# Kernel tuning notes

Hardware: AMD Instinct MI355X
Metric: run time of the kernel (lower is better)

The kernel has to match this reference:

```python
import jax, jax.numpy as jnp
import numpy as np


def setup_inputs() -> dict:
    key = jax.random.key(0)
    ks = jax.random.split(key, 13)
    B, T, D = 512, 256, 64
    H, G = 256, 192          # encoder hidden, lifted dim
    L = D + G                # ldim = 256
    s = lambda n: 1.0 / np.sqrt(n)
    return {
        "x": jax.random.normal(ks[0], (B, T, D), jnp.float32),
        "u": jax.random.normal(ks[1], (B, T, D), jnp.float32),
        "Wx1": jax.random.normal(ks[2], (D, H), jnp.float32) * s(D),
        "bx1": jax.random.normal(ks[3], (H,), jnp.float32) * 0.01,
        "Wx2": jax.random.normal(ks[4], (H, H), jnp.float32) * s(H),
        "bx2": jax.random.normal(ks[5], (H,), jnp.float32) * 0.01,
        "Wx3": jax.random.normal(ks[6], (H, G), jnp.float32) * s(H),
        "Wu1": jax.random.normal(ks[7], (D, H), jnp.float32) * s(D),
        "bu1": jax.random.normal(ks[8], (H,), jnp.float32) * 0.01,
        "Wu2": jax.random.normal(ks[9], (H, G), jnp.float32) * s(H),
        "WB": jax.random.normal(ks[10], (D + G, L), jnp.float32) * s(D + G),
        "WK": jax.random.normal(ks[11], (L, L), jnp.float32) * s(L),
        "bK": jax.random.normal(ks[12], (L,), jnp.float32) * 0.01,
        "n_shifts": 256,
    }


def reference(x, u, Wx1, bx1, Wx2, bx2, Wx3, Wu1, bu1, Wu2, WB, WK, bK, n_shifts):
    x = x[:, :n_shifts, :]
    u = u[:, :n_shifts, :]
    # encoder_x: relu(Linear) -> relu(Linear) -> Linear(no bias), dropout p=0 is identity
    g = jnp.maximum(x @ Wx1 + bx1, 0.0)
    g = jnp.maximum(g @ Wx2 + bx2, 0.0)
    g = g @ Wx3
    y = jnp.concatenate([x, g], axis=-1)          # [B, T, ldim]
    # encoder_u: relu(Linear) -> Linear(no bias)
    v = jnp.maximum(u @ Wu1 + bu1, 0.0) @ Wu2
    uu = jnp.concatenate([u, v], axis=-1)         # [B, T, D+G]
    Bu = uu @ WB                                  # [B, T, ldim]
    # Koopman linear recurrence: y_{t+1} = K y_t + bK + Bu_t
    y0 = y[:, 0, :]                               # [B, ldim]

    def step(carry, bu_t):
        y_next = carry @ WK + bK + bu_t
        return y_next, y_next

    _, ys = jax.lax.scan(step, y0, jnp.swapaxes(Bu[:, :-1, :], 0, 1))  # [T-1, B, ldim]
    y_pred = jnp.concatenate([y0[:, None, :], jnp.swapaxes(ys, 0, 1)], axis=1)
    return (y, y_pred)
```

## Files before the change

kernel.cpp:

```cpp
#include <hip/hip_runtime.h>
#include <hip/hip_bf16.h>

#define MM 131072

typedef __attribute__((ext_vector_type(8))) short short8;
typedef __attribute__((ext_vector_type(4))) float f32x4;

#define GLP(p) (const __attribute__((address_space(1))) void*)(p)
#define LDSP(p) (__attribute__((address_space(3))) void*)(p)

static __device__ __forceinline__ unsigned short f2bf(float f) {
    union { float f; unsigned int u; } v; v.f = f;
    unsigned int r = v.u + 0x7FFF + ((v.u >> 16) & 1);
    return (unsigned short)(r >> 16);
}
static __device__ __forceinline__ float bf2f(unsigned short h) {
    union { float f; unsigned int u; } v; v.u = ((unsigned int)h) << 16;
    return v.f;
}

__global__ __launch_bounds__(256) void prepA(
    const float* __restrict__ x, const float* __restrict__ u,
    __hip_bfloat16* __restrict__ xb, __hip_bfloat16* __restrict__ ub,
    float* __restrict__ y,
    const float* __restrict__ W0, const float* __restrict__ W1,
    const float* __restrict__ W2, const float* __restrict__ W3,
    const float* __restrict__ W4, const float* __restrict__ W5,
    __hip_bfloat16* __restrict__ T0, __hip_bfloat16* __restrict__ T1,
    __hip_bfloat16* __restrict__ T2, __hip_bfloat16* __restrict__ T3,
    __hip_bfloat16* __restrict__ T4, __hip_bfloat16* __restrict__ T5,
    const float* __restrict__ WK, const float* __restrict__ WB,
    float* __restrict__ W2f, float* __restrict__ WBWf)
{
    __shared__ __align__(16) float As[16][68];
    __shared__ __align__(16) float Ws[16][64];

    if (blockIdx.x < 16384) {
        int i = blockIdx.x * 256 + threadIdx.x;
        const float* s; __hip_bfloat16* d; int j; bool isx;
        if (i < 2097152) { s = x; d = xb; j = i; isx = true; }
        else             { s = u; d = ub; j = i - 2097152; isx = false; }
        const float4 v = ((const float4*)s)[j];
        union { unsigned short h[4]; uint2 u2; } p;
        p.h[0] = f2bf(v.x); p.h[1] = f2bf(v.y);
        p.h[2] = f2bf(v.z); p.h[3] = f2bf(v.w);
        ((uint2*)d)[j] = p.u2;
        if (isx) {
            const int r = j >> 4, q = j & 15;
            ((float4*)(y + (size_t)r * 256))[q] = v;
        }
    } else if (blockIdx.x < 17408) {
        const int b = blockIdx.x - 16384;
        const float* W; __hip_bfloat16* T; int K, N, i0;
        if      (b < 64)  { W = W0; T = T0; K = 64;  N = 256; i0 = b; }
        else if (b < 320) { W = W1; T = T1; K = 256; N = 256; i0 = b - 64; }
        else if (b < 512) { W = W2; T = T2; K = 256; N = 192; i0 = b - 320; }
        else if (b < 576) { W = W3; T = T3; K = 64;  N = 256; i0 = b - 512; }
        else if (b < 768) { W = W4; T = T4; K = 256; N = 192; i0 = b - 576; }
        else              { W = W5; T = T5; K = 256; N = 256; i0 = b - 768; }
        const int i = i0 * 256 + threadIdx.x;
        if (i < K * N) {
            const int n = i / K, k = i - n * K;
            T[i] = __float2bfloat16(W[(size_t)k * N + n]);
        }
    } else {
        const int tile = blockIdx.x - 17408;
        const int e  = tile >> 4;
        const int tl = tile & 15;
        const float* A = e ? WB : WK;
        const float* W = WK;
        float*       C = e ? WBWf : W2f;
        const int row0 = (tl >> 2) * 64;
        const int col0 = (tl & 3) * 64;
        const int tx = threadIdx.x & 15;
        const int ty = threadIdx.x >> 4;
        float acc[4][4] = {};
        for (int k0 = 0; k0 < 256; k0 += 16) {
            {
                const int kk = threadIdx.x & 15;
                const int r  = threadIdx.x >> 4;
                #pragma unroll
                for (int rr = 0; rr < 4; ++rr)
                    As[kk][r + rr * 16] = A[(size_t)(row0 + r + rr * 16) * 256 + k0 + kk];
            }
            {
                const int n  = threadIdx.x & 63;
                const int kz = threadIdx.x >> 6;
                #pragma unroll
                for (int kq = 0; kq < 4; ++kq) {
                    const int kk = kz + kq * 4;
                    Ws[kk][n] = W[(size_t)(k0 + kk) * 256 + col0 + n];
                }
            }
            __syncthreads();
            #pragma unroll
            for (int kk = 0; kk < 16; ++kk) {
                const float4 a4 = *(const float4*)&As[kk][ty * 4];
                const float4 w4 = *(const float4*)&Ws[kk][tx * 4];
                const float av[4] = {a4.x, a4.y, a4.z, a4.w};
                const float wv[4] = {w4.x, w4.y, w4.z, w4.w};
                #pragma unroll
                for (int i = 0; i < 4; ++i)
                    #pragma unroll
                    for (int j = 0; j < 4; ++j)
                        acc[i][j] += av[i] * wv[j];
            }
            __syncthreads();
        }
        #pragma unroll
        for (int i = 0; i < 4; ++i)
            #pragma unroll
            for (int j = 0; j < 4; ++j)
                C[(size_t)(row0 + ty * 4 + i) * 256 + col0 + tx * 4 + j] = acc[i][j];
    }
}

struct G5 { const float* a[5]; const float* b[5]; float* c[5]; };

__global__ __launch_bounds__(256) void wgemm(G5 P)
{
    __shared__ __align__(16) float As[16][68];
    __shared__ __align__(16) float Ws[16][64];

    const int e  = blockIdx.x >> 4;
    const int tl = blockIdx.x & 15;
    const float* A = P.a[e];
    const float* W = P.b[e];
    float*       C = P.c[e];
    const int row0 = (tl >> 2) * 64;
    const int col0 = (tl & 3) * 64;

    const int tx = threadIdx.x & 15;
    const int ty = threadIdx.x >> 4;

    float acc[4][4] = {};

    for (int k0 = 0; k0 < 256; k0 += 16) {
        {
            const int kk = threadIdx.x & 15;
            const int r  = threadIdx.x >> 4;
            #pragma unroll
            for (int rr = 0; rr < 4; ++rr)
                As[kk][r + rr * 16] = A[(size_t)(row0 + r + rr * 16) * 256 + k0 + kk];
        }
        {
            const int n  = threadIdx.x & 63;
            const int kz = threadIdx.x >> 6;
            #pragma unroll
            for (int kq = 0; kq < 4; ++kq) {
                const int kk = kz + kq * 4;
                Ws[kk][n] = W[(size_t)(k0 + kk) * 256 + col0 + n];
            }
        }
        __syncthreads();
        #pragma unroll
        for (int kk = 0; kk < 16; ++kk) {
            const float4 a4 = *(const float4*)&As[kk][ty * 4];
            const float4 w4 = *(const float4*)&Ws[kk][tx * 4];
            const float av[4] = {a4.x, a4.y, a4.z, a4.w};
            const float wv[4] = {w4.x, w4.y, w4.z, w4.w};
            #pragma unroll
            for (int i = 0; i < 4; ++i)
                #pragma unroll
                for (int j = 0; j < 4; ++j)
                    acc[i][j] += av[i] * wv[j];
        }
        __syncthreads();
    }

    #pragma unroll
    for (int i = 0; i < 4; ++i)
        #pragma unroll
        for (int j = 0; j < 4; ++j)
            C[(size_t)(row0 + ty * 4 + i) * 256 + col0 + tx * 4 + j] = acc[i][j];
}

__global__ __launch_bounds__(512) void ffC(
    const __hip_bfloat16* __restrict__ x_bf,
    const __hip_bfloat16* __restrict__ u_bf,
    const __hip_bfloat16* __restrict__ Wx1T, const float* __restrict__ bx1,
    const __hip_bfloat16* __restrict__ Wx2T, const float* __restrict__ bx2,
    const __hip_bfloat16* __restrict__ Wx3T,
    const __hip_bfloat16* __restrict__ Wu1T, const float* __restrict__ bu1,
    const __hip_bfloat16* __restrict__ Wu2T,
    float* __restrict__ y, __hip_bfloat16* __restrict__ vout,
    const float* __restrict__ WB, const float* __restrict__ WBW,
    const float* __restrict__ WBW2, const float* __restrict__ WBW3,
    __hip_bfloat16* __restrict__ T4,
    const float* __restrict__ bK, const float* __restrict__ WK,
    const float* __restrict__ W2f, const float* __restrict__ W3f,
    float* __restrict__ cK4)
{
    __shared__ __align__(16) __hip_bfloat16 I[128 * 256];
    __shared__ __align__(16) __hip_bfloat16 Bs[256 * 32];
    __shared__ __align__(16) __hip_bfloat16 As[128 * 32];

    const int tid  = threadIdx.x;

    if (blockIdx.x >= 2048) {
        if (blockIdx.x < 2560) {
            const int o = (blockIdx.x - 2048) * 512 + tid;
            const int n = o >> 10;
            const int rem = o & 1023;
            const int j = rem >> 8, k = rem & 255;
            const float* src = (j == 0) ? WB : (j == 1) ? WBW : (j == 2) ? WBW2 : WBW3;
            ((unsigned short*)T4)[o] = f2bf(src[(size_t)k * 256 + n]);
        } else {
            if (tid < 256) {
                const int col = tid;
                float s = bK[col];
                for (int k = 0; k < 256; ++k)
                    s += bK[k] * (WK[(size_t)k * 256 + col] + W2f[(size_t)k * 256 + col]
                                  + W3f[(size_t)k * 256 + col]);
                cK4[col] = s;
            }
        }
        return;
    }

    const bool isx = blockIdx.x < 1024;
    const __hip_bfloat16* in  = isx ? x_bf : u_bf;
    const __hip_bfloat16* W1T = isx ? Wx1T : Wu1T;
    const float*          b1  = isx ? bx1  : bu1;
    const int lane = tid & 63;
    const int wid  = tid >> 6;
    const int wm   = wid & 1;
    const int wn   = wid >> 1;
    const int row0 = (blockIdx.x & 1023) * 128;
    const int rlow = lane & 15;
    const int c    = lane >> 4;

    f32x4 acc[4][4];
    #pragma unroll
    for (int mi = 0; mi < 4; ++mi)
        #pragma unroll
        for (int ni = 0; ni < 4; ++ni)
            acc[mi][ni] = {0.f, 0.f, 0.f, 0.f};

    for (int k0 = 0; k0 < 64; k0 += 32) {
        {
            const int i = tid;
            const int row = i >> 2;
            const int cl  = (i & 3) ^ ((row >> 1) & 3);
            __builtin_amdgcn_global_load_lds(
                GLP(in + (size_t)(row0 + row) * 64 + k0 + cl * 8),
                LDSP(As + i * 8), 16, 0, 0);
        }
        #pragma unroll
        for (int r = 0; r < 2; ++r) {
            const int i = r * 512 + tid;
            const int row = i >> 2;
            const int cl  = (i & 3) ^ ((row >> 1) & 3);
            __builtin_amdgcn_global_load_lds(
                GLP(W1T + (size_t)row * 64 + k0 + cl * 8),
                LDSP(Bs + i * 8), 16, 0, 0);
        }
        __syncthreads();
        short8 af[4], bfr[4];
        #pragma unroll
        for (int mi = 0; mi < 4; ++mi) {
            const int row  = wm * 64 + mi * 16 + rlow;
            const int phys = c ^ ((row >> 1) & 3);
            af[mi] = *(const short8*)((const char*)As + row * 64 + phys * 16);
        }
        #pragma unroll
        for (int ni = 0; ni < 4; ++ni) {
            const int row  = wn * 64 + ni * 16 + rlow;
            const int phys = c ^ ((row >> 1) & 3);
            bfr[ni] = *(const short8*)((const char*)Bs + row * 64 + phys * 16);
        }
        #pragma unroll
        for (int mi = 0; mi < 4; ++mi)
            #pragma unroll
            for (int ni = 0; ni < 4; ++ni)
                acc[mi][ni] = __builtin_amdgcn_mfma_f32_16x16x32_bf16(
                    af[mi], bfr[ni], acc[mi][ni], 0, 0, 0);
        __syncthreads();
    }
    #pragma unroll
    for (int ni = 0; ni < 4; ++ni) {
        const int col = wn * 64 + ni * 16 + rlow;
        const float bv = b1[col];
        #pragma unroll
        for (int mi = 0; mi < 4; ++mi)
            #pragma unroll
            for (int q = 0; q < 4; ++q) {
                const int row = wm * 64 + mi * 16 + c * 4 + q;
                const int byte = (row * 512 + col * 2) ^ ((row & 7) << 4);
                *(unsigned short*)((char*)I + byte) = f2bf(fmaxf(acc[mi][ni][q] + bv, 0.f));
            }
    }
    __syncthreads();

    if (isx) {
        #pragma unroll
        for (int mi = 0; mi < 4; ++mi)
            #pragma unroll
            for (int ni = 0; ni < 4; ++ni)
                acc[mi][ni] = {0.f, 0.f, 0.f, 0.f};

        for (int k0 = 0; k0 < 256; k0 += 32) {
            #pragma unroll
            for (int r = 0; r < 2; ++r) {
                const int i = r * 512 + tid;
                const int row = i >> 2;
                const int cl  = (i & 3) ^ ((row >> 1) & 3);
                __builtin_amdgcn_global_load_lds(
                    GLP(Wx2T + (size_t)row * 256 + k0 + cl * 8),
                    LDSP(Bs + i * 8), 16, 0, 0);
            }
            __syncthreads();
            short8 af[4], bfr[4];
            #pragma unroll
            for (int mi = 0; mi < 4; ++mi) {
                const int row = wm * 64 + mi * 16 + rlow;
                const int off = (row * 512 + k0 * 2 + c * 16) ^ ((row & 7) << 4);
                af[mi] = *(const short8*)((const char*)I + off);
            }
            #pragma unroll
            for (int ni = 0; ni < 4; ++ni) {
                const int row  = wn * 64 + ni * 16 + rlow;
                const int phys = c ^ ((row >> 1) & 3);
                bfr[ni] = *(const short8*)((const char*)Bs + row * 64 + phys * 16);
            }
            #pragma unroll
            for (int mi = 0; mi < 4; ++mi)
                #pragma unroll
                for (int ni = 0; ni < 4; ++ni)
                    acc[mi][ni] = __builtin_amdgcn_mfma_f32_16x16x32_bf16(
                        af[mi], bfr[ni], acc[mi][ni], 0, 0, 0);
            __syncthreads();
        }
        #pragma unroll
        for (int ni = 0; ni < 4; ++ni) {
            const int col = wn * 64 + ni * 16 + rlow;
            const float bv = bx2[col];
            #pragma unroll
            for (int mi = 0; mi < 4; ++mi)
                #pragma unroll
                for (int q = 0; q < 4; ++q) {
                    const int row = wm * 64 + mi * 16 + c * 4 + q;
                    const int byte = (row * 512 + col * 2) ^ ((row & 7) << 4);
                    *(unsigned short*)((char*)I + byte) = f2bf(fmaxf(acc[mi][ni][q] + bv, 0.f));
                }
        }
        __syncthreads();
    }

    const __hip_bfloat16* WfT = isx ? Wx3T : Wu2T;
    f32x4 a3[4][3];
    #pragma unroll
    for (int mi = 0; mi < 4; ++mi)
        #pragma unroll
        for (int ni = 0; ni < 3; ++ni)
            a3[mi][ni] = {0.f, 0.f, 0.f, 0.f};

    for (int k0 = 0; k0 < 256; k0 += 32) {
        #pragma unroll
        for (int r = 0; r < 2; ++r) {
            const int i = r * 512 + tid;
            if (i < 768) {
                const int row = i >> 2;
                const int cl  = (i & 3) ^ ((row >> 1) & 3);
                __builtin_amdgcn_global_load_lds(
                    GLP(WfT + (size_t)row * 256 + k0 + cl * 8),
                    LDSP(Bs + i * 8), 16, 0, 0);
            }
        }
        __syncthreads();
        short8 af[4], bfr[3];
        #pragma unroll
        for (int mi = 0; mi < 4; ++mi) {
            const int row = wm * 64 + mi * 16 + rlow;
            const int off = (row * 512 + k0 * 2 + c * 16) ^ ((row & 7) << 4);
            af[mi] = *(const short8*)((const char*)I + off);
        }
        #pragma unroll
        for (int ni = 0; ni < 3; ++ni) {
            const int row  = wn * 48 + ni * 16 + rlow;
            const int phys = c ^ ((row >> 1) & 3);
            bfr[ni] = *(const short8*)((const char*)Bs + row * 64 + phys * 16);
        }
        #pragma unroll
        for (int mi = 0; mi < 4; ++mi)
            #pragma unroll
            for (int ni = 0; ni < 3; ++ni)
                a3[mi][ni] = __builtin_amdgcn_mfma_f32_16x16x32_bf16(
                    af[mi], bfr[ni], a3[mi][ni], 0, 0, 0);
        __syncthreads();
    }
    #pragma unroll
    for (int ni = 0; ni < 3; ++ni) {
        const int col = wn * 48 + ni * 16 + rlow;
        #pragma unroll
        for (int mi = 0; mi < 4; ++mi)
            #pragma unroll
            for (int q = 0; q < 4; ++q) {
                const int row = row0 + wm * 64 + mi * 16 + c * 4 + q;
                if (isx) y[(size_t)row * 256 + 64 + col] = a3[mi][ni][q];
                else     ((unsigned short*)vout)[(size_t)row * 192 + col] = f2bf(a3[mi][ni][q]);
            }
    }
}

__global__ __launch_bounds__(256) void d4gS(
    const __hip_bfloat16* __restrict__ u_bf, const __hip_bfloat16* __restrict__ v,
    const __hip_bfloat16* __restrict__ WBT4, const float* __restrict__ cK4,
    float* __restrict__ yp,
    const __hip_bfloat16* __restrict__ WBT, const float* __restrict__ bK,
    float* __restrict__ stash)
{
    __shared__ __align__(16) __hip_bfloat16 As[132 * 32];
    __shared__ __align__(16) __hip_bfloat16 Bs[4][128 * 32];

    const int tid  = threadIdx.x;

    if (blockIdx.x >= 2048) {
        float* uuL = (float*)As;
        const int b = blockIdx.x - 2048;
        #pragma unroll
        for (int p = 0; p < 3; ++p) {
            float val;
            if (tid < 64) val = bf2f(((const unsigned short*)u_bf)[((size_t)b * 256 + p) * 64 + tid]);
            else          val = bf2f(((const unsigned short*)v)[((size_t)b * 256 + p) * 192 + tid - 64]);
            uuL[p * 256 + tid] = val;
        }
        __syncthreads();
        const int col = tid;
        float a0 = bK[col], a1 = a0, a2 = a0;
        for (int k = 0; k < 256; ++k) {
            const float w = bf2f(((const unsigned short*)WBT)[(size_t)col * 256 + k]);
            a0 += uuL[0 * 256 + k] * w;
            a1 += uuL[1 * 256 + k] * w;
            a2 += uuL[2 * 256 + k] * w;
        }
        stash[((size_t)b * 3 + 0) * 256 + col] = a0;
        stash[((size_t)b * 3 + 1) * 256 + col] = a1;
        stash[((size_t)b * 3 + 2) * 256 + col] = a2;
        return;
    }

    const int lane = tid & 63;
    const int wid  = tid >> 6;
    const int wm   = wid & 1;
    const int wn   = wid >> 1;
    const int row0 = (blockIdx.x >> 1) * 128;
    const int col0 = (blockIdx.x & 1) * 128;
    const int rlow = lane & 15;
    const int c    = lane >> 4;

    f32x4 acc[4][4];
    #pragma unroll
    for (int mi = 0; mi < 4; ++mi)
        #pragma unroll
        for (int ni = 0; ni < 4; ++ni)
            acc[mi][ni] = {0.f, 0.f, 0.f, 0.f};

    for (int kl = 0; kl < 256; kl += 32) {
        const __hip_bfloat16* Ab; int Al, kk;
        if (kl < 64) { Ab = u_bf; Al = 64;  kk = kl; }
        else         { Ab = v;    Al = 192; kk = kl - 64; }

        #pragma unroll
        for (int r = 0; r < 3; ++r) {
            const int i = r * 256 + tid;
            if (i < 528) {
                const int row = i >> 2;
                const int cl  = (i & 3) ^ ((row >> 1) & 3);
                int srow = row0 - 4 + row;
                if (srow < 0) srow = 0;
                __builtin_amdgcn_global_load_lds(
                    GLP(Ab + (size_t)srow * Al + kk + cl * 8),
                    LDSP(As + i * 8), 16, 0, 0);
            }
        }
        #pragma unroll
        for (int r = 0; r < 8; ++r) {
            const int i = r * 256 + tid;
            const int j = i >> 9;
            const int s = i & 511;
            const int row = s >> 2;
            const int cl  = (s & 3) ^ ((row >> 1) & 3);
            __builtin_amdgcn_global_load_lds(
                GLP(WBT4 + (size_t)(col0 + row) * 1024 + j * 256 + kl + cl * 8),
                LDSP(&Bs[0][0] + i * 8), 16, 0, 0);
        }
        __syncthreads();

        #pragma unroll
        for (int j = 0; j < 4; ++j) {
            short8 bfr[4];
            #pragma unroll
            for (int ni = 0; ni < 4; ++ni) {
                const int row  = wn * 64 + ni * 16 + rlow;
                const int phys = c ^ ((row >> 1) & 3);
                bfr[ni] = *(const short8*)((const char*)Bs[j] + row * 64 + phys * 16);
            }
            #pragma unroll
            for (int mi = 0; mi < 4; ++mi) {
                const int prow = wm * 64 + mi * 16 + rlow + 3 - j;
                const int phys = c ^ ((prow >> 1) & 3);
                const short8 af = *(const short8*)((const char*)As + prow * 64 + phys * 16);
                #pragma unroll
                for (int ni = 0; ni < 4; ++ni)
                    acc[mi][ni] = __builtin_amdgcn_mfma_f32_16x16x32_bf16(
                        af, bfr[ni], acc[mi][ni], 0, 0, 0);
            }
        }
        __syncthreads();
    }

    const int q4 = lane >> 4;
    #pragma unroll
    for (int ni = 0; ni < 4; ++ni) {
        const int col = col0 + wn * 64 + ni * 16 + rlow;
        const float bv = cK4[col];
        #pragma unroll
        for (int mi = 0; mi < 4; ++mi) {
            #pragma unroll
            for (int q = 0; q < 4; ++q) {
                const int row = row0 + wm * 64 + mi * 16 + q4 * 4 + q;
                if ((row & 255) >= 4)
                    yp[(size_t)row * 256 + col] = acc[mi][ni][q] + bv;
            }
        }
    }
}

static __device__ __forceinline__ void gather_frags(
    const float* __restrict__ M, int col0, int rlow, int kg,
    short8 (&wh)[2][8], short8 (&wl)[2][8])
{
    #pragma unroll
    for (int tile = 0; tile < 2; ++tile) {
        const int col = col0 + tile * 16 + rlow;
        for (int kc = 0; kc < 8; ++kc) {
            const int k0 = kc * 32 + kg * 8;
            short8 h, l;
            for (int i = 0; i < 8; ++i) {
                const float w = M[(size_t)(k0 + i) * 256 + col];
                const unsigned short hb = f2bf(w);
                h[i] = (short)hb;
                l[i] = (short)f2bf(w - bf2f(hb));
            }
            wh[tile][kc] = h;
            wl[tile][kc] = l;
        }
    }
}

__global__ __launch_bounds__(512, 1) void scan4(
    const float* __restrict__ WK, const float* __restrict__ W4,
    const float* __restrict__ stash,
    const float* __restrict__ y, float* __restrict__ yp)
{
    __shared__ __align__(16) __hip_bfloat16 cbuf[2][2][16 * 256];

    const int tid  = threadIdx.x;
    const int lane = tid & 63;
    const int wid  = tid >> 6;
    const int b0   = blockIdx.x * 4;
    const int col0 = wid * 32;
    const int rlow = lane & 15;
    const int kg   = lane >> 4;
    const int rswz = (rlow & 7) << 4;

    #pragma unroll
    for (int e = 0; e < 2; ++e) {
        const int idx = tid * 2 + e;
        const int br  = idx >> 8;
        const int cc  = idx & 255;
        const float v = y[(size_t)(b0 + br) * 65536 + cc];
        yp[(size_t)(b0 + br) * 65536 + cc] = v;
        const unsigned short hb = f2bf(v);
        const unsigned short lb = f2bf(v - bf2f(hb));
        const int byte = (br * 512 + cc * 2) ^ ((br & 7) << 4);
        *(unsigned short*)((char*)&cbuf[0][0][0] + byte) = hb;
        *(unsigned short*)((char*)&cbuf[0][1][0] + byte) = lb;
    }
    __syncthreads();

    short8 wh[2][8], wl[2][8];
    gather_frags(WK, col0, rlow, kg, wh, wl);

    for (int p = 1; p < 4; ++p) {
        f32x4 aHH[2], aHL[2], aLH[2];
        #pragma unroll
        for (int tile = 0; tile < 2; ++tile) {
            aHH[tile] = {0.f, 0.f, 0.f, 0.f};
            aHL[tile] = {0.f, 0.f, 0.f, 0.f};
            aLH[tile] = {0.f, 0.f, 0.f, 0.f};
        }
        const char* hbase = (const char*)&cbuf[0][0][0];
        const char* lbase = (const char*)&cbuf[0][1][0];
        #pragma unroll
        for (int kc = 0; kc < 8; ++kc) {
            const int off = (rlow * 512 + kg * 16 + kc * 64) ^ rswz;
            const short8 ah = *(const short8*)(hbase + off);
            const short8 al = *(const short8*)(lbase + off);
            aHH[0] = __builtin_amdgcn_mfma_f32_16x16x32_bf16(ah, wh[0][kc], aHH[0], 0, 0, 0);
            aHH[1] = __builtin_amdgcn_mfma_f32_16x16x32_bf16(ah, wh[1][kc], aHH[1], 0, 0, 0);
            aHL[0] = __builtin_amdgcn_mfma_f32_16x16x32_bf16(ah, wl[0][kc], aHL[0], 0, 0, 0);
            aHL[1] = __builtin_amdgcn_mfma_f32_16x16x32_bf16(ah, wl[1][kc], aHL[1], 0, 0, 0);
            aLH[0] = __builtin_amdgcn_mfma_f32_16x16x32_bf16(al, wh[0][kc], aLH[0], 0, 0, 0);
            aLH[1] = __builtin_amdgcn_mfma_f32_16x16x32_bf16(al, wh[1][kc], aLH[1], 0, 0, 0);
        }
        __builtin_amdgcn_sched_barrier(0);
        asm volatile("s_waitcnt lgkmcnt(0)" ::: "memory");
        __builtin_amdgcn_s_barrier();
        __builtin_amdgcn_sched_barrier(0);

        if (kg == p - 1) {
            #pragma unroll
            for (int tile = 0; tile < 2; ++tile) {
                const int col = col0 + tile * 16 + rlow;
                #pragma unroll
                for (int q = 0; q < 4; ++q) {
                    const float cv = stash[((size_t)(b0 + q) * 3 + (p - 1)) * 256 + col];
                    const float yv = aHH[tile][q] + aHL[tile][q] + aLH[tile][q] + cv;
                    const int wr = p * 4 + q;
                    const unsigned short hb = f2bf(yv);
                    const unsigned short lb = f2bf(yv - bf2f(hb));
                    const int byte = (wr * 512 + col * 2) ^ ((wr & 7) << 4);
                    *(unsigned short*)((char*)&cbuf[0][0][0] + byte) = hb;
                    *(unsigned short*)((char*)&cbuf[0][1][0] + byte) = lb;
                    yp[(size_t)(b0 + q) * 65536 + (size_t)p * 256 + col] = yv;
                }
            }
        }
        __builtin_amdgcn_sched_barrier(0);
        asm volatile("s_waitcnt lgkmcnt(0)" ::: "memory");
        __builtin_amdgcn_s_barrier();
        __builtin_amdgcn_sched_barrier(0);
    }

    gather_frags(W4, col0, rlow, kg, wh, wl);

    float dv[2][4];
    #pragma unroll
    for (int tile = 0; tile < 2; ++tile) {
        const int col = col0 + tile * 16 + rlow;
        #pragma unroll
        for (int q = 0; q < 4; ++q)
            dv[tile][q] = yp[(size_t)(b0 + q) * 65536 + (size_t)(4 + kg) * 256 + col];
    }

    int cur = 0;
    for (int s = 0; s < 63; ++s) {
        const int tb = 4 + s * 4;

        float dn[2][4];
        if (s < 62) {
            #pragma unroll
            for (int tile = 0; tile < 2; ++tile) {
                const int col = col0 + tile * 16 + rlow;
                #pragma unroll
                for (int q = 0; q < 4; ++q)
                    dn[tile][q] = yp[(size_t)(b0 + q) * 65536
                                     + (size_t)(tb + 4 + kg) * 256 + col];
            }
        }

        f32x4 aHH[2], aHL[2], aLH[2];
        #pragma unroll
        for (int tile = 0; tile < 2; ++tile) {
            aHH[tile] = {0.f, 0.f, 0.f, 0.f};
            aHL[tile] = {0.f, 0.f, 0.f, 0.f};
            aLH[tile] = {0.f, 0.f, 0.f, 0.f};
        }
        const char* hbase = (const char*)&cbuf[cur][0][0];
        const char* lbase = (const char*)&cbuf[cur][1][0];
        #pragma unroll
        for (int kc = 0; kc < 8; ++kc) {
            const int off = (rlow * 512 + kg * 16 + kc * 64) ^ rswz;
            const short8 ah = *(const short8*)(hbase + off);
            const short8 al = *(const short8*)(lbase + off);
            aHH[0] = __builtin_amdgcn_mfma_f32_16x16x32_bf16(ah, wh[0][kc], aHH[0], 0, 0, 0);
            aHH[1] = __builtin_amdgcn_mfma_f32_16x16x32_bf16(ah, wh[1][kc], aHH[1], 0, 0, 0);
            aHL[0] = __builtin_amdgcn_mfma_f32_16x16x32_bf16(ah, wl[0][kc], aHL[0], 0, 0, 0);
            aHL[1] = __builtin_amdgcn_mfma_f32_16x16x32_bf16(ah, wl[1][kc], aHL[1], 0, 0, 0);
            aLH[0] = __builtin_amdgcn_mfma_f32_16x16x32_bf16(al, wh[0][kc], aLH[0], 0, 0, 0);
            aLH[1] = __builtin_amdgcn_mfma_f32_16x16x32_bf16(al, wh[1][kc], aLH[1], 0, 0, 0);
        }

        char* whb = (char*)&cbuf[cur ^ 1][0][0];
        char* wlb = (char*)&cbuf[cur ^ 1][1][0];
        #pragma unroll
        for (int tile = 0; tile < 2; ++tile) {
            const int col = col0 + tile * 16 + rlow;
            #pragma unroll
            for (int q = 0; q < 4; ++q) {
                const int row = kg * 4 + q;
                const float yv = aHH[tile][q] + aHL[tile][q] + aLH[tile][q] + dv[tile][q];
                const unsigned short hb = f2bf(yv);
                const unsigned short lb = f2bf(yv - bf2f(hb));
                const int byte = (row * 512 + col * 2) ^ ((row & 7) << 4);
                *(unsigned short*)(whb + byte) = hb;
                *(unsigned short*)(wlb + byte) = lb;
                yp[(size_t)(b0 + q) * 65536 + (size_t)(tb + kg) * 256 + col] = yv;
            }
        }
        if (s < 62) {
            #pragma unroll
            for (int tile = 0; tile < 2; ++tile)
                #pragma unroll
                for (int q = 0; q < 4; ++q)
                    dv[tile][q] = dn[tile][q];
        }

        __builtin_amdgcn_sched_barrier(0);
        asm volatile("s_waitcnt lgkmcnt(0)" ::: "memory");
        __builtin_amdgcn_s_barrier();
        __builtin_amdgcn_sched_barrier(0);
        cur ^= 1;
    }
}

extern "C" void kernel_launch(void* const* d_in, const int* in_sizes, int n_in,
                              void* d_out, int out_size, void* d_ws, size_t ws_size,
                              hipStream_t stream)
{
    const float* x   = (const float*)d_in[0];
    const float* u   = (const float*)d_in[1];
    const float* Wx1 = (const float*)d_in[2];
    const float* bx1 = (const float*)d_in[3];
    const float* Wx2 = (const float*)d_in[4];
    const float* bx2 = (const float*)d_in[5];
    const float* Wx3 = (const float*)d_in[6];
    const float* Wu1 = (const float*)d_in[7];
    const float* bu1 = (const float*)d_in[8];
    const float* Wu2 = (const float*)d_in[9];
    const float* WB  = (const float*)d_in[10];
    const float* WK  = (const float*)d_in[11];
    const float* bK  = (const float*)d_in[12];

    float* y  = (float*)d_out;
    float* yp = y + (size_t)MM * 256;

    char* ws = (char*)d_ws;
    __hip_bfloat16* x_bf = (__hip_bfloat16*)(ws);
    __hip_bfloat16* u_bf = (__hip_bfloat16*)(ws + 16777216);
    __hip_bfloat16* wTb  = (__hip_bfloat16*)(ws + 33554432);
    __hip_bfloat16* Wx1T = wTb;
    __hip_bfloat16* Wx2T = wTb + 16384;
    __hip_bfloat16* Wx3T = wTb + 81920;
    __hip_bfloat16* Wu1T = wTb + 131072;
    __hip_bfloat16* Wu2T = wTb + 147456;
    __hip_bfloat16* WBT  = wTb + 196608;
    __hip_bfloat16* t2   = (__hip_bfloat16*)(ws + 34078720);
    float* W2f   = (float*)(ws + 101187584);
    float* W3f   = (float*)(ws + 101449728);
    float* W4f   = (float*)(ws + 101711872);
    float* WBWf  = (float*)(ws + 101974016);
    float* WBW2f = (float*)(ws + 102236160);
    float* WBW3f = (float*)(ws + 102498304);
    __hip_bfloat16* WBT4 = (__hip_bfloat16*)(ws + 102760448);
    float* cK4   = (float*)(ws + 103284736);
    float* stash = (float*)(ws + 103285760);

    prepA<<<17440, dim3(256), 0, stream>>>(x, u, x_bf, u_bf, y,
        Wx1, Wx2, Wx3, Wu1, Wu2, WB,
        Wx1T, Wx2T, Wx3T, Wu1T, Wu2T, WBT,
        WK, WB, W2f, WBWf);

    {
        G5 L2 = {{W2f, W2f, WBWf, WBWf, nullptr},
                 {WK, W2f, WK, W2f, nullptr},
                 {W3f, W4f, WBW2f, WBW3f, nullptr}};
        wgemm<<<64, dim3(256), 0, stream>>>(L2);
    }

    ffC<<<2561, dim3(512), 0, stream>>>(x_bf, u_bf,
        Wx1T, bx1, Wx2T, bx2, Wx3T, Wu1T, bu1, Wu2T,
        y, t2,
        WB, WBWf, WBW2f, WBW3f, WBT4,
        bK, WK, W2f, W3f, cK4);

    d4gS<<<2560, dim3(256), 0, stream>>>(u_bf, t2, WBT4, cK4, yp, WBT, bK, stash);

    scan4<<<128, dim3(512), 0, stream>>>(WK, W4f, stash, y, yp);
}
```

Measured before the change: 410.3 us.

## Load larger K tiles in encoder MLP and split recurrence MFMA accumulator chains

```diff
diff --git a/kernel.cpp b/kernel.cpp
--- a/kernel.cpp
+++ b/kernel.cpp
@@ -192,8 +192,8 @@
     float* __restrict__ cK4)
 {
     __shared__ __align__(16) __hip_bfloat16 I[128 * 256];
-    __shared__ __align__(16) __hip_bfloat16 Bs[256 * 32];
-    __shared__ __align__(16) __hip_bfloat16 As[128 * 32];
+    __shared__ __align__(16) __hip_bfloat16 Bs[256 * 128];
+    __shared__ __align__(16) __hip_bfloat16 As[128 * 64];
 
     const int tid  = threadIdx.x;
 
@@ -237,91 +237,40 @@
         for (int ni = 0; ni < 4; ++ni)
             acc[mi][ni] = {0.f, 0.f, 0.f, 0.f};
 
-    for (int k0 = 0; k0 < 64; k0 += 32) {
-        {
-            const int i = tid;
-            const int row = i >> 2;
-            const int cl  = (i & 3) ^ ((row >> 1) & 3);
-            __builtin_amdgcn_global_load_lds(
-                GLP(in + (size_t)(row0 + row) * 64 + k0 + cl * 8),
-                LDSP(As + i * 8), 16, 0, 0);
-        }
+    {
         #pragma unroll
         for (int r = 0; r < 2; ++r) {
             const int i = r * 512 + tid;
-            const int row = i >> 2;
-            const int cl  = (i & 3) ^ ((row >> 1) & 3);
+            const int row = i >> 3;
+            const int cl  = (i & 7) ^ (row & 7);
             __builtin_amdgcn_global_load_lds(
-                GLP(W1T + (size_t)row * 64 + k0 + cl * 8),
+                GLP(in + (size_t)(row0 + row) * 64 + cl * 8),
+                LDSP(As + i * 8), 16, 0, 0);
+        }
+        #pragma unroll
+        for (int r = 0; r < 4; ++r) {
+            const int i = r * 512 + tid;
+            const int row = i >> 3;
+            const int cl  = (i & 7) ^ (row & 7);
+            __builtin_amdgcn_global_load_lds(
+                GLP(W1T + (size_t)row * 64 + cl * 8),
                 LDSP(Bs + i * 8), 16, 0, 0);
         }
         __syncthreads();
-        short8 af[4], bfr[4];
-        #pragma unroll
-        for (int mi = 0; mi < 4; ++mi) {
-            const int row  = wm * 64 + mi * 16 + rlow;
-            const int phys = c ^ ((row >> 1) & 3);
-            af[mi] = *(const short8*)((const char*)As + row * 64 + phys * 16);
-        }
-        #pragma unroll
-        for (int ni = 0; ni < 4; ++ni) {
-            const int row  = wn * 64 + ni * 16 + rlow;
-            const int phys = c ^ ((row >> 1) & 3);
-            bfr[ni] = *(const short8*)((const char*)Bs + row * 64 + phys * 16);
-        }
-        #pragma unroll
-        for (int mi = 0; mi < 4; ++mi)
-            #pragma unroll
-            for (int ni = 0; ni < 4; ++ni)
-                acc[mi][ni] = __builtin_amdgcn_mfma_f32_16x16x32_bf16(
-                    af[mi], bfr[ni], acc[mi][ni], 0, 0, 0);
-        __syncthreads();
-    }
-    #pragma unroll
-    for (int ni = 0; ni < 4; ++ni) {
-        const int col = wn * 64 + ni * 16 + rlow;
-        const float bv = b1[col];
-        #pragma unroll
-        for (int mi = 0; mi < 4; ++mi)
-            #pragma unroll
-            for (int q = 0; q < 4; ++q) {
-                const int row = wm * 64 + mi * 16 + c * 4 + q;
-                const int byte = (row * 512 + col * 2) ^ ((row & 7) << 4);
-                *(unsigned short*)((char*)I + byte) = f2bf(fmaxf(acc[mi][ni][q] + bv, 0.f));
-            }
-    }
-    __syncthreads();
-
-    if (isx) {
-        #pragma unroll
-        for (int mi = 0; mi < 4; ++mi)
-            #pragma unroll
-            for (int ni = 0; ni < 4; ++ni)
-                acc[mi][ni] = {0.f, 0.f, 0.f, 0.f};
-
-        for (int k0 = 0; k0 < 256; k0 += 32) {
-            #pragma unroll
-            for (int r = 0; r < 2; ++r) {
-                const int i = r * 512 + tid;
-                const int row = i >> 2;
-                const int cl  = (i & 3) ^ ((row >> 1) & 3);
-                __builtin_amdgcn_global_load_lds(
-                    GLP(Wx2T + (size_t)row * 256 + k0 + cl * 8),
-                    LDSP(Bs + i * 8), 16, 0, 0);
-            }
-            __syncthreads();
+        #pragma unroll
+        for (int k0 = 0; k0 < 64; k0 += 32) {
             short8 af[4], bfr[4];
             #pragma unroll
             for (int mi = 0; mi < 4; ++mi) {
-                const int row = wm * 64 + mi * 16 + rlow;
-                const int off = (row * 512 + k0 * 2 + c * 16) ^ ((row & 7) << 4);
-                af[mi] = *(const short8*)((const char*)I + off);
+                const int row  = wm * 64 + mi * 16 + rlow;
+                const int phys = ((k0 >> 3) + c) ^ (row & 7);
+                af[mi] = *(const short8*)((const char*)As + row * 128 + phys * 16);
             }
             #pragma unroll
             for (int ni = 0; ni < 4; ++ni) {
                 const int row  = wn * 64 + ni * 16 + rlow;
-                const int phys = c ^ ((row >> 1) & 3);
-                bfr[ni] = *(const short8*)((const char*)Bs + row * 64 + phys * 16);
+                const int phys = ((k0 >> 3) + c) ^ (row & 7);
+                bfr[ni] = *(const short8*)((const char*)Bs + row * 128 + phys * 16);
             }
             #pragma unroll
             for (int mi = 0; mi < 4; ++mi)
@@ -329,16 +278,16 @@
                 for (int ni = 0; ni < 4; ++ni)
                     acc[mi][ni] = __builtin_amdgcn_mfma_f32_16x16x32_bf16(
                         af[mi], bfr[ni], acc[mi][ni], 0, 0, 0);
-            __syncthreads();
-        }
+        }
+        __syncthreads();
         #pragma unroll
         for (int ni = 0; ni < 4; ++ni) {
             const int col = wn * 64 + ni * 16 + rlow;
-            const float bv = bx2[col];
-            #pragma unroll
-            for (int mi = 0; mi < 4; ++mi)
-                #pragma unroll
-                for (int q = 0; q < 4; ++q) {
+            const float bv = b1[col];
+            #pragma unroll
+            for (int q = 0; q < 4; ++q)
+                #pragma unroll
+                for (int mi = 0; mi < 4; ++mi) {
                     const int row = wm * 64 + mi * 16 + c * 4 + q;
                     const int byte = (row * 512 + col * 2) ^ ((row & 7) << 4);
                     *(unsigned short*)((char*)I + byte) = f2bf(fmaxf(acc[mi][ni][q] + bv, 0.f));
@@ -347,6 +296,65 @@
         __syncthreads();
     }
 
+    if (isx) {
+        #pragma unroll
+        for (int mi = 0; mi < 4; ++mi)
+            #pragma unroll
+            for (int ni = 0; ni < 4; ++ni)
+                acc[mi][ni] = {0.f, 0.f, 0.f, 0.f};
+
+        for (int half = 0; half < 2; ++half) {
+            const int k0b = half * 128;
+            #pragma unroll
+            for (int r = 0; r < 8; ++r) {
+                const int i = r * 512 + tid;
+                const int row = i >> 4;
+                const int cl  = (i & 15) ^ (row & 7);
+                __builtin_amdgcn_global_load_lds(
+                    GLP(Wx2T + (size_t)row * 256 + k0b + cl * 8),
+                    LDSP(Bs + i * 8), 16, 0, 0);
+            }
+            __syncthreads();
+            #pragma unroll
+            for (int k0l = 0; k0l < 128; k0l += 32) {
+                short8 af[4], bfr[4];
+                #pragma unroll
+                for (int mi = 0; mi < 4; ++mi) {
+                    const int row = wm * 64 + mi * 16 + rlow;
+                    const int off = (row * 512 + (k0b + k0l) * 2 + c * 16) ^ ((row & 7) << 4);
+                    af[mi] = *(const short8*)((const char*)I + off);
+                }
+                #pragma unroll
+                for (int ni = 0; ni < 4; ++ni) {
+                    const int row  = wn * 64 + ni * 16 + rlow;
+                    const int phys = ((k0l >> 3) + c) ^ (row & 7);
+                    bfr[ni] = *(const short8*)((const char*)Bs + row * 256 + phys * 16);
+                }
+                #pragma unroll
+                for (int mi = 0; mi < 4; ++mi)
+                    #pragma unroll
+                    for (int ni = 0; ni < 4; ++ni)
+                        acc[mi][ni] = __builtin_amdgcn_mfma_f32_16x16x32_bf16(
+                            af[mi], bfr[ni], acc[mi][ni], 0, 0, 0);
+            }
+            __syncthreads();
+        }
+        #pragma unroll
+        for (int ni = 0; ni < 4; ++ni) {
+            const int col = wn * 64 + ni * 16 + rlow;
+            const float bv = bx2[col];
+            #pragma unroll
+            for (int q = 0; q < 4; ++q)
+                #pragma unroll
+                for (int mi = 0; mi < 4; ++mi) {
+                    const int row = wm * 64 + mi * 16 + c * 4 + q;
+                    const int byte = (row * 512 + col * 2) ^ ((row & 7) << 4);
+                    *(unsigned short*)((char*)I + byte) = f2bf(fmaxf(acc[mi][ni][q] + bv, 0.f));
+                }
+        }
+        __syncthreads();
+    }
+
     const __hip_bfloat16* WfT = isx ? Wx3T : Wu2T;
     f32x4 a3[4][3];
     #pragma unroll
@@ -355,38 +363,40 @@
         for (int ni = 0; ni < 3; ++ni)
             a3[mi][ni] = {0.f, 0.f, 0.f, 0.f};
 
-    for (int k0 = 0; k0 < 256; k0 += 32) {
-        #pragma unroll
-        for (int r = 0; r < 2; ++r) {
+    for (int half = 0; half < 2; ++half) {
+        const int k0b = half * 128;
+        #pragma unroll
+        for (int r = 0; r < 6; ++r) {
             const int i = r * 512 + tid;
-            if (i < 768) {
-                const int row = i >> 2;
-                const int cl  = (i & 3) ^ ((row >> 1) & 3);
-                __builtin_amdgcn_global_load_lds(
-                    GLP(WfT + (size_t)row * 256 + k0 + cl * 8),
-                    LDSP(Bs + i * 8), 16, 0, 0);
-            }
-        }
-        __syncthreads();
-        short8 af[4], bfr[3];
-        #pragma unroll
-        for (int mi = 0; mi < 4; ++mi) {
-            const int row = wm * 64 + mi * 16 + rlow;
-            const int off = (row * 512 + k0 * 2 + c * 16) ^ ((row & 7) << 4);
-            af[mi] = *(const short8*)((const char*)I + off);
-        }
-        #pragma unroll
-        for (int ni = 0; ni < 3; ++ni) {
-            const int row  = wn * 48 + ni * 16 + rlow;
-            const int phys = c ^ ((row >> 1) & 3);
-            bfr[ni] = *(const short8*)((const char*)Bs + row * 64 + phys * 16);
-        }
-        #pragma unroll
-        for (int mi = 0; mi < 4; ++mi)
-            #pragma unroll
-            for (int ni = 0; ni < 3; ++ni)
-                a3[mi][ni] = __builtin_amdgcn_mfma_f32_16x16x32_bf16(
-                    af[mi], bfr[ni], a3[mi][ni], 0, 0, 0);
+            const int row = i >> 4;
+            const int cl  = (i & 15) ^ (row & 7);
+            __builtin_amdgcn_global_load_lds(
+                GLP(WfT + (size_t)row * 256 + k0b + cl * 8),
+                LDSP(Bs + i * 8), 16, 0, 0);
+        }
+        __syncthreads();
+        #pragma unroll
+        for (int k0l = 0; k0l < 128; k0l += 32) {
+            short8 af[4], bfr[3];
+            #pragma unroll
+            for (int mi = 0; mi < 4; ++mi) {
+                const int row = wm * 64 + mi * 16 + rlow;
+                const int off = (row * 512 + (k0b + k0l) * 2 + c * 16) ^ ((row & 7) << 4);
+                af[mi] = *(const short8*)((const char*)I + off);
+            }
+            #pragma unroll
+            for (int ni = 0; ni < 3; ++ni) {
+                const int row  = wn * 48 + ni * 16 + rlow;
+                const int phys = ((k0l >> 3) + c) ^ (row & 7);
+                bfr[ni] = *(const short8*)((const char*)Bs + row * 256 + phys * 16);
+            }
+            #pragma unroll
+            for (int mi = 0; mi < 4; ++mi)
+                #pragma unroll
+                for (int ni = 0; ni < 3; ++ni)
+                    a3[mi][ni] = __builtin_amdgcn_mfma_f32_16x16x32_bf16(
+                        af[mi], bfr[ni], a3[mi][ni], 0, 0, 0);
+        }
         __syncthreads();
     }
     #pragma unroll
@@ -584,17 +594,16 @@
     gather_frags(WK, col0, rlow, kg, wh, wl);
 
     for (int p = 1; p < 4; ++p) {
-        f32x4 aHH[2], aHL[2], aLH[2];
+        f32x4 aHH[2], aHL[2], aLH[2], bHH[2], bHL[2], bLH[2];
         #pragma unroll
         for (int tile = 0; tile < 2; ++tile) {
-            aHH[tile] = {0.f, 0.f, 0.f, 0.f};
-            aHL[tile] = {0.f, 0.f, 0.f, 0.f};
-            aLH[tile] = {0.f, 0.f, 0.f, 0.f};
+            aHH[tile] = {0.f,0.f,0.f,0.f}; aHL[tile] = {0.f,0.f,0.f,0.f}; aLH[tile] = {0.f,0.f,0.f,0.f};
+            bHH[tile] = {0.f,0.f,0.f,0.f}; bHL[tile] = {0.f,0.f,0.f,0.f}; bLH[tile] = {0.f,0.f,0.f,0.f};
         }
         const char* hbase = (const char*)&cbuf[0][0][0];
         const char* lbase = (const char*)&cbuf[0][1][0];
         #pragma unroll
-        for (int kc = 0; kc < 8; ++kc) {
+        for (int kc = 0; kc < 4; ++kc) {
             const int off = (rlow * 512 + kg * 16 + kc * 64) ^ rswz;
             const short8 ah = *(const short8*)(hbase + off);
             const short8 al = *(const short8*)(lbase + off);
@@ -605,6 +614,18 @@
             aLH[0] = __builtin_amdgcn_mfma_f32_16x16x32_bf16(al, wh[0][kc], aLH[0], 0, 0, 0);
             aLH[1] = __builtin_amdgcn_mfma_f32_16x16x32_bf16(al, wh[1][kc], aLH[1], 0, 0, 0);
         }
+        #pragma unroll
+        for (int kc = 4; kc < 8; ++kc) {
+            const int off = (rlow * 512 + kg * 16 + kc * 64) ^ rswz;
+            const short8 ah = *(const short8*)(hbase + off);
+            const short8 al = *(const short8*)(lbase + off);
+            bHH[0] = __builtin_amdgcn_mfma_f32_16x16x32_bf16(ah, wh[0][kc], bHH[0], 0, 0, 0);
+            bHH[1] = __builtin_amdgcn_mfma_f32_16x16x32_bf16(ah, wh[1][kc], bHH[1], 0, 0, 0);
+            bHL[0] = __builtin_amdgcn_mfma_f32_16x16x32_bf16(ah, wl[0][kc], bHL[0], 0, 0, 0);
+            bHL[1] = __builtin_amdgcn_mfma_f32_16x16x32_bf16(ah, wl[1][kc], bHL[1], 0, 0, 0);
+            bLH[0] = __builtin_amdgcn_mfma_f32_16x16x32_bf16(al, wh[0][kc], bLH[0], 0, 0, 0);
+            bLH[1] = __builtin_amdgcn_mfma_f32_16x16x32_bf16(al, wh[1][kc], bLH[1], 0, 0, 0);
+        }
         __builtin_amdgcn_sched_barrier(0);
         asm volatile("s_waitcnt lgkmcnt(0)" ::: "memory");
         __builtin_amdgcn_s_barrier();
@@ -617,7 +638,8 @@
                 #pragma unroll
                 for (int q = 0; q < 4; ++q) {
                     const float cv = stash[((size_t)(b0 + q) * 3 + (p - 1)) * 256 + col];
-                    const float yv = aHH[tile][q] + aHL[tile][q] + aLH[tile][q] + cv;
+                    const float yv = (aHH[tile][q] + bHH[tile][q]) + (aHL[tile][q] + bHL[tile][q])
+                                   + (aLH[tile][q] + bLH[tile][q]) + cv;
                     const int wr = p * 4 + q;
                     const unsigned short hb = f2bf(yv);
                     const unsigned short lb = f2bf(yv - bf2f(hb));
@@ -661,17 +683,16 @@
             }
         }
 
-        f32x4 aHH[2], aHL[2], aLH[2];
+        f32x4 aHH[2], aHL[2], aLH[2], bHH[2], bHL[2], bLH[2];
         #pragma unroll
         for (int tile = 0; tile < 2; ++tile) {
-            aHH[tile] = {0.f, 0.f, 0.f, 0.f};
-            aHL[tile] = {0.f, 0.f, 0.f, 0.f};
-            aLH[tile] = {0.f, 0.f, 0.f, 0.f};
+            aHH[tile] = {0.f,0.f,0.f,0.f}; aHL[tile] = {0.f,0.f,0.f,0.f}; aLH[tile] = {0.f,0.f,0.f,0.f};
+            bHH[tile] = {0.f,0.f,0.f,0.f}; bHL[tile] = {0.f,0.f,0.f,0.f}; bLH[tile] = {0.f,0.f,0.f,0.f};
         }
         const char* hbase = (const char*)&cbuf[cur][0][0];
         const char* lbase = (const char*)&cbuf[cur][1][0];
         #pragma unroll
-        for (int kc = 0; kc < 8; ++kc) {
+        for (int kc = 0; kc < 4; ++kc) {
             const int off = (rlow * 512 + kg * 16 + kc * 64) ^ rswz;
             const short8 ah = *(const short8*)(hbase + off);
             const short8 al = *(const short8*)(lbase + off);
@@ -682,6 +703,18 @@
             aLH[0] = __builtin_amdgcn_mfma_f32_16x16x32_bf16(al, wh[0][kc], aLH[0], 0, 0, 0);
             aLH[1] = __builtin_amdgcn_mfma_f32_16x16x32_bf16(al, wh[1][kc], aLH[1], 0, 0, 0);
         }
+        #pragma unroll
+        for (int kc = 4; kc < 8; ++kc) {
+            const int off = (rlow * 512 + kg * 16 + kc * 64) ^ rswz;
+            const short8 ah = *(const short8*)(hbase + off);
+            const short8 al = *(const short8*)(lbase + off);
+            bHH[0] = __builtin_amdgcn_mfma_f32_16x16x32_bf16(ah, wh[0][kc], bHH[0], 0, 0, 0);
+            bHH[1] = __builtin_amdgcn_mfma_f32_16x16x32_bf16(ah, wh[1][kc], bHH[1], 0, 0, 0);
+            bHL[0] = __builtin_amdgcn_mfma_f32_16x16x32_bf16(ah, wl[0][kc], bHL[0], 0, 0, 0);
+            bHL[1] = __builtin_amdgcn_mfma_f32_16x16x32_bf16(ah, wl[1][kc], bHL[1], 0, 0, 0);
+            bLH[0] = __builtin_amdgcn_mfma_f32_16x16x32_bf16(al, wh[0][kc], bLH[0], 0, 0, 0);
+            bLH[1] = __builtin_amdgcn_mfma_f32_16x16x32_bf16(al, wh[1][kc], bLH[1], 0, 0, 0);
+        }
 
         char* whb = (char*)&cbuf[cur ^ 1][0][0];
         char* wlb = (char*)&cbuf[cur ^ 1][1][0];
@@ -691,7 +724,8 @@
             #pragma unroll
             for (int q = 0; q < 4; ++q) {
                 const int row = kg * 4 + q;
-                const float yv = aHH[tile][q] + aHL[tile][q] + aLH[tile][q] + dv[tile][q];
+                const float yv = (aHH[tile][q] + bHH[tile][q]) + (aHL[tile][q] + bHL[tile][q])
+                               + (aLH[tile][q] + bLH[tile][q]) + dv[tile][q];
                 const unsigned short hb = f2bf(yv);
                 const unsigned short lb = f2bf(yv - bf2f(hb));
                 const int byte = (row * 512 + col * 2) ^ ((row & 7) << 4);
```

Result: faster. 392.7 us (-4.3%).
